# Kernel optimization log

Measured on AMD Instinct MI355X. Metric: run time of the kernel, lower is better.

The kernel has to match this reference:

```python
import jax, jax.numpy as jnp
import numpy as np

DIM = 128
KNN = 16
EPS = 1e-5


def knn_feature(coords, k):
    # coords: [B, K, D]; returns [B, K, k] nearest-neighbor indices (self excluded)
    inner = -2.0 * jnp.einsum('bid,bjd->bij', coords, coords)
    xx = jnp.sum(coords * coords, axis=-1, keepdims=True)  # [B,K,1]
    dist = xx + jnp.swapaxes(xx, 1, 2) + inner  # [B,K,K]
    K = coords.shape[1]
    diag = jnp.eye(K, dtype=bool)[None]
    dist = jnp.where(diag, 1e9, dist)
    _, idx = jax.lax.top_k(-dist, k)  # smallest distances
    return idx


def setup_inputs() -> dict:
    key = jax.random.key(0)
    ks = jax.random.split(key, 10)
    B, K, C = 8, 4096, DIM
    s1 = 1.0 / np.sqrt(2 * C)
    s2 = 1.0 / np.sqrt(C)
    return {
        'x': jax.random.normal(ks[0], (B, K, C), jnp.float32),
        'pos_embed': jax.random.normal(ks[1], (B, K, C), jnp.float32),
        'rel_pos_coords': jax.random.normal(ks[2], (B, K, 3), jnp.float32),
        'gamma': jnp.ones((C,), jnp.float32),
        'beta': jnp.zeros((C,), jnp.float32),
        'W_a1': jax.random.normal(ks[3], (2 * C, C), jnp.float32) * s1,
        'b_a1': jnp.zeros((C,), jnp.float32),
        'W_a2': jax.random.normal(ks[4], (C, 1), jnp.float32) * s2,
        'b_a2': jnp.zeros((1,), jnp.float32),
        'W_f1': jax.random.normal(ks[5], (2 * C, C), jnp.float32) * s1,
        'b_f1': jnp.zeros((C,), jnp.float32),
    }


def reference(x, pos_embed, rel_pos_coords, gamma, beta, W_a1, b_a1, W_a2, b_a2, W_f1, b_f1):
    B, K, C = x.shape
    k_eff = min(KNN, K - 1)
    # Pre-norm LayerNorm + positional embedding
    mu = jnp.mean(x, axis=-1, keepdims=True)
    var = jnp.mean((x - mu) ** 2, axis=-1, keepdims=True)
    x_norm = (x - mu) * jax.lax.rsqrt(var + EPS) * gamma + beta
    xp = x_norm + pos_embed  # [B,K,C]

    idx = knn_feature(rel_pos_coords, k_eff)  # [B,K,k]
    neighbor_feat = jax.vmap(lambda f, i: f[i])(xp, idx)  # [B,K,k,C]
    self_feat = jnp.broadcast_to(xp[:, :, None, :], neighbor_feat.shape)

    attn_in = jnp.concatenate([self_feat, neighbor_feat], axis=-1)  # [B,K,k,2C]
    h = jax.nn.leaky_relu(attn_in @ W_a1 + b_a1, 0.2)
    logits = h @ W_a2 + b_a2  # [B,K,k,1]
    attn = jax.nn.softmax(logits, axis=2)

    feat_in = jnp.concatenate([self_feat, neighbor_feat - self_feat], axis=-1)
    transformed = jax.nn.leaky_relu(feat_in @ W_f1 + b_f1, 0.2)  # [B,K,k,C]

    agg = jnp.sum(attn * transformed, axis=2)  # [B,K,C]
    # DropPath in eval mode is identity
    return agg
```

## Files before the change

kernel.cpp:

```cpp
#include <hip/hip_runtime.h>

#define B_ 8
#define K_ 4096
#define C_ 128
#define KN 16

typedef __attribute__((ext_vector_type(8))) short bf16x8;
typedef __attribute__((ext_vector_type(4))) float f32x4;

__device__ __forceinline__ unsigned short f2bf(float f) {
  unsigned u = __float_as_uint(f);
  unsigned r = (u + 0x7FFFu + ((u >> 16) & 1u)) >> 16;
  return (unsigned short)r;
}
__device__ __forceinline__ float bf2f(unsigned short s) {
  return __uint_as_float(((unsigned)s) << 16);
}

__device__ __forceinline__ float dist_exact(float4 q, float4 c) {
  float dot = __fadd_rn(__fadd_rn(__fmul_rn(q.x, c.x), __fmul_rn(q.y, c.y)),
                        __fmul_rn(q.z, c.z));
  return __fadd_rn(__fadd_rn(q.w, c.w), __fmul_rn(-2.0f, dot));
}
__device__ __forceinline__ float escr(float4 q, float4 c, float ch) {
  return fmaf(-q.x, c.x, fmaf(-q.y, c.y, fmaf(-q.z, c.z, ch)));
}

__global__ __launch_bounds__(256) void k_pre(
    const float* __restrict__ x, const float* __restrict__ pos,
    const float* __restrict__ gamma, const float* __restrict__ beta,
    const float* __restrict__ Wa1, const float* __restrict__ Wf1,
    const float* __restrict__ coords, unsigned short* __restrict__ A,
    unsigned short* __restrict__ WT, float4* __restrict__ cc4) {
  int blk = blockIdx.x;
  if (blk < 8192) {
    int wave = threadIdx.x >> 6;
    int lane = threadIdx.x & 63;
    size_t row = (size_t)blk * 4 + wave;
    const float2* xr = (const float2*)(x + row * C_);
    const float2* pr = (const float2*)(pos + row * C_);
    float2 a = xr[lane];
    float s = a.x + a.y;
#pragma unroll
    for (int o = 1; o < 64; o <<= 1) s += __shfl_xor(s, o);
    float mu = s * (1.0f / 128.0f);
    float dx = a.x - mu, dy = a.y - mu;
    float v = dx * dx + dy * dy;
#pragma unroll
    for (int o = 1; o < 64; o <<= 1) v += __shfl_xor(v, o);
    float rstd = rsqrtf(v * (1.0f / 128.0f) + 1e-5f);
    float2 gm = ((const float2*)gamma)[lane];
    float2 bt = ((const float2*)beta)[lane];
    float2 pp = pr[lane];
    float o0 = dx * rstd * gm.x + bt.x + pp.x;
    float o1 = dy * rstd * gm.y + bt.y + pp.y;
    ushort2 o = make_ushort2(f2bf(o0), f2bf(o1));
    *(ushort2*)(A + row * C_ + 2 * lane) = o;
  } else if (blk < 8320) {
    int i = (blk - 8192) * 256 + threadIdx.x;
    float px = coords[i * 3], py = coords[i * 3 + 1], pz = coords[i * 3 + 2];
    float w = __fadd_rn(__fadd_rn(__fmul_rn(px, px), __fmul_rn(py, py)),
                        __fmul_rn(pz, pz));
    cc4[i] = make_float4(px, py, pz, w);
  } else {
    int i = (blk - 8320) * 256 + threadIdx.x;
    int q = i >> 7;
    int r = i & 127;
    float v;
    if (q < 128)
      v = Wa1[r * 128 + q];
    else if (q < 256)
      v = Wf1[r * 128 + (q - 128)] - Wf1[(128 + r) * 128 + (q - 128)];
    else {
      int c = (q - 256) >> 1;
      if (((q - 256) & 1) == 0)
        v = Wa1[(128 + r) * 128 + c];
      else
        v = Wf1[(128 + r) * 128 + c];
    }
    WT[i] = f2bf(v);
  }
}

__global__ __launch_bounds__(256) void k_knn(const float4* __restrict__ cc4,
                                             int* __restrict__ idx) {
  __shared__ unsigned cbuf[4][4][64];
  __shared__ unsigned scnt[4][4];
  int wave = threadIdx.x >> 6, lane = threadIdx.x & 63;
  int gw = blockIdx.x * 4 + wave;
  int b = gw >> 10;
  int qbase = (gw & 1023) * 4;
  const float4* cb = cc4 + (size_t)b * K_;
  if (lane < 4) scnt[wave][lane] = 0u;
  __asm__ volatile("s_waitcnt lgkmcnt(0)" ::: "memory");
  float4 Q[4];
#pragma unroll
  for (int qq = 0; qq < 4; ++qq) Q[qq] = cb[qbase + qq];

  float m0 = 1e30f, m1 = 1e30f, m2 = 1e30f, m3 = 1e30f;
#pragma unroll 4
  for (int it = 0; it < 48; ++it) {
    float4 c = cb[(it << 6) + lane];
    float ch = c.w * 0.5f;
    m0 = fminf(m0, escr(Q[0], c, ch));
    m1 = fminf(m1, escr(Q[1], c, ch));
    m2 = fminf(m2, escr(Q[2], c, ch));
    m3 = fminf(m3, escr(Q[3], c, ch));
  }
  float ub[4];
  float mv[4] = {m0, m1, m2, m3};
#pragma unroll
  for (int qq = 0; qq < 4; ++qq) {
    float v = mv[qq];
#pragma unroll
    for (int k = 2; k <= 64; k <<= 1) {
#pragma unroll
      for (int jj = k >> 1; jj >= 1; jj >>= 1) {
        float o = __shfl_xor(v, jj);
        bool amHigh = (lane & jj) != 0;
        bool up = (lane & k) != 0;
        bool gt = v > o;
        bool take = (amHigh ? !gt : gt) ^ up;
        v = take ? o : v;
      }
    }
    ub[qq] = __shfl(v, 16) + 5e-4f;
  }

#pragma unroll 2
  for (int it = 0; it < 64; ++it) {
    int j = (it << 6) + lane;
    float4 c = cb[j];
    float ch = c.w * 0.5f;
#pragma unroll
    for (int qq = 0; qq < 4; ++qq) {
      float e = escr(Q[qq], c, ch);
      if (e <= ub[qq]) {
        unsigned pos = atomicAdd(&scnt[wave][qq], 1u);
        if (pos < 64u) cbuf[wave][qq][pos] = (unsigned)j;
      }
    }
  }
  __asm__ volatile("s_waitcnt lgkmcnt(0)" ::: "memory");

#pragma unroll
  for (int qq = 0; qq < 4; ++qq) {
    unsigned m = scnt[wave][qq];
    m = m < 64u ? m : 64u;
    bool valid = lane < (int)m;
    unsigned ji = valid ? cbuf[wave][qq][lane] : 0u;
    if (valid && ji == (unsigned)(qbase + qq)) valid = false;
    float4 c = cb[ji];
    float dC = valid ? dist_exact(Q[qq], c) : 1e30f;
    int iC = valid ? (int)ji : 0x7fffffff;
#pragma unroll
    for (int k = 2; k <= 64; k <<= 1) {
#pragma unroll
      for (int jj = k >> 1; jj >= 1; jj >>= 1) {
        float od = __shfl_xor(dC, jj);
        int oi = __shfl_xor(iC, jj);
        bool amHigh = (lane & jj) != 0;
        bool up = (lane & k) != 0;
        bool gt = (dC > od) || (dC == od && iC > oi);
        bool take = (amHigh ? !gt : gt) ^ up;
        dC = take ? od : dC;
        iC = take ? oi : iC;
      }
    }
    if (lane < KN)
      idx[((size_t)b * K_ + (qbase + qq)) * KN + lane] = iC;
  }
}

__global__ __launch_bounds__(256) void k_gemm_mfma(
    const unsigned short* __restrict__ A, const unsigned short* __restrict__ BT,
    unsigned short* __restrict__ SN) {
  __shared__ char lB[32768];
  int bb = blockIdx.x & 7;
  int rest = blockIdx.x >> 3;
  int mbl = rest >> 2, nb = rest & 3;
  int m0 = bb * 4096 + mbl * 128, n0 = nb * 128;
  int t = threadIdx.x;
  {
    const char* src = (const char*)(BT + (size_t)n0 * 128);
#pragma unroll
    for (int i = 0; i < 8; ++i) {
      int byte = (t + i * 256) * 16;
      int n = byte >> 8;
      int sb = byte ^ ((n & 7) << 4);
      *(float4*)(lB + sb) = *(const float4*)(src + byte);
    }
  }
  __syncthreads();
  int wave = t >> 6, lane = t & 63;
  int wr = wave >> 1, wc = wave & 1;
  int lm = lane & 15, lk = lane >> 4;
  f32x4 z = {0.f, 0.f, 0.f, 0.f};
  f32x4 acc00 = z, acc01 = z, acc02 = z, acc03 = z;
  f32x4 acc10 = z, acc11 = z, acc12 = z, acc13 = z;
  f32x4 acc20 = z, acc21 = z, acc22 = z, acc23 = z;
  f32x4 acc30 = z, acc31 = z, acc32 = z, acc33 = z;
  const char* abase =
      (const char*)A + (size_t)(m0 + wr * 64 + lm) * 256 + lk * 16;
#pragma unroll
  for (int ks = 0; ks < 4; ++ks) {
    bf16x8 af[4], bfr[4];
#pragma unroll
    for (int mt = 0; mt < 4; ++mt)
      af[mt] = *(const bf16x8*)(abase + (size_t)mt * 4096 + ks * 64);
#pragma unroll
    for (int nt = 0; nt < 4; ++nt) {
      int n_local = wc * 64 + nt * 16 + lm;
      int byte = n_local * 256 + ks * 64 + lk * 16;
      byte ^= (n_local & 7) << 4;
      bfr[nt] = *(const bf16x8*)(lB + byte);
    }
    acc00 = __builtin_amdgcn_mfma_f32_16x16x32_bf16(af[0], bfr[0], acc00, 0, 0, 0);
    acc01 = __builtin_amdgcn_mfma_f32_16x16x32_bf16(af[0], bfr[1], acc01, 0, 0, 0);
    acc02 = __builtin_amdgcn_mfma_f32_16x16x32_bf16(af[0], bfr[2], acc02, 0, 0, 0);
    acc03 = __builtin_amdgcn_mfma_f32_16x16x32_bf16(af[0], bfr[3], acc03, 0, 0, 0);
    acc10 = __builtin_amdgcn_mfma_f32_16x16x32_bf16(af[1], bfr[0], acc10, 0, 0, 0);
    acc11 = __builtin_amdgcn_mfma_f32_16x16x32_bf16(af[1], bfr[1], acc11, 0, 0, 0);
    acc12 = __builtin_amdgcn_mfma_f32_16x16x32_bf16(af[1], bfr[2], acc12, 0, 0, 0);
    acc13 = __builtin_amdgcn_mfma_f32_16x16x32_bf16(af[1], bfr[3], acc13, 0, 0, 0);
    acc20 = __builtin_amdgcn_mfma_f32_16x16x32_bf16(af[2], bfr[0], acc20, 0, 0, 0);
    acc21 = __builtin_amdgcn_mfma_f32_16x16x32_bf16(af[2], bfr[1], acc21, 0, 0, 0);
    acc22 = __builtin_amdgcn_mfma_f32_16x16x32_bf16(af[2], bfr[2], acc22, 0, 0, 0);
    acc23 = __builtin_amdgcn_mfma_f32_16x16x32_bf16(af[2], bfr[3], acc23, 0, 0, 0);
    acc30 = __builtin_amdgcn_mfma_f32_16x16x32_bf16(af[3], bfr[0], acc30, 0, 0, 0);
    acc31 = __builtin_amdgcn_mfma_f32_16x16x32_bf16(af[3], bfr[1], acc31, 0, 0, 0);
    acc32 = __builtin_amdgcn_mfma_f32_16x16x32_bf16(af[3], bfr[2], acc32, 0, 0, 0);
    acc33 = __builtin_amdgcn_mfma_f32_16x16x32_bf16(af[3], bfr[3], acc33, 0, 0, 0);
  }
  f32x4 accs[4][4] = {{acc00, acc01, acc02, acc03},
                      {acc10, acc11, acc12, acc13},
                      {acc20, acc21, acc22, acc23},
                      {acc30, acc31, acc32, acc33}};
#pragma unroll
  for (int mt = 0; mt < 4; ++mt) {
#pragma unroll
    for (int nt = 0; nt < 4; ++nt) {
#pragma unroll
      for (int r = 0; r < 4; ++r) {
        int row = m0 + wr * 64 + mt * 16 + lk * 4 + r;
        int col = n0 + wc * 64 + nt * 16 + lm;
        SN[(size_t)row * 512 + col] = f2bf(accs[mt][nt][r]);
      }
    }
  }
}

__global__ __launch_bounds__(256) void k_attn(
    const unsigned short* __restrict__ SN, const int* __restrict__ idx,
    const float* __restrict__ b_a1, const float* __restrict__ b_f1,
    const float* __restrict__ W_a2, const float* __restrict__ b_a2,
    float* __restrict__ out) {
  int wave = threadIdx.x >> 6, lane = threadIdx.x & 63;
  int g = lane >> 4, r = lane & 15;
  int b = blockIdx.x & 7;
  int w = blockIdx.x >> 3;
  size_t gpt = (size_t)b * K_ + w * 4 + wave;
  const unsigned short* sr = SN + gpt * 512;
  bf16x8 sa8 = *(const bf16x8*)(sr + 8 * r);
  bf16x8 sf8 = *(const bf16x8*)(sr + 128 + 8 * r);
  float4 bav0 = *(const float4*)(b_a1 + 8 * r);
  float4 bav1 = *(const float4*)(b_a1 + 8 * r + 4);
  float4 bfv0 = *(const float4*)(b_f1 + 8 * r);
  float4 bfv1 = *(const float4*)(b_f1 + 8 * r + 4);
  float4 w2v0 = *(const float4*)(W_a2 + 8 * r);
  float4 w2v1 = *(const float4*)(W_a2 + 8 * r + 4);
  float sab[8], sfb[8], w2v[8];
  {
    float bav[8] = {bav0.x, bav0.y, bav0.z, bav0.w, bav1.x, bav1.y, bav1.z, bav1.w};
    float bfv[8] = {bfv0.x, bfv0.y, bfv0.z, bfv0.w, bfv1.x, bfv1.y, bfv1.z, bfv1.w};
    float wv[8] = {w2v0.x, w2v0.y, w2v0.z, w2v0.w, w2v1.x, w2v1.y, w2v1.z, w2v1.w};
#pragma unroll
    for (int i = 0; i < 8; ++i) {
      sab[i] = bf2f((unsigned short)sa8[i]) + bav[i];
      sfb[i] = bf2f((unsigned short)sf8[i]) + bfv[i];
      w2v[i] = wv[i];
    }
  }
  float ba2v = b_a2[0];
  int nv = 0;
  if (lane < 16) nv = idx[gpt * 16 + lane];
  float lgl[4];
  float tsv[4][8];
#pragma unroll
  for (int round = 0; round < 4; ++round) {
    int n = __shfl(nv, round * 4 + g);
    const unsigned short* nr =
        SN + ((size_t)b * K_ + n) * 512 + 256 + 16 * r;
    bf16x8 u0 = *(const bf16x8*)(nr);
    bf16x8 u1 = *(const bf16x8*)(nr + 8);
    float dot = 0.0f;
#pragma unroll
    for (int i = 0; i < 4; ++i) {
      float h = sab[i] + bf2f((unsigned short)u0[2 * i]);
      h = h >= 0.0f ? h : 0.2f * h;
      float tv = sfb[i] + bf2f((unsigned short)u0[2 * i + 1]);
      tv = tv >= 0.0f ? tv : 0.2f * tv;
      dot = fmaf(h, w2v[i], dot);
      tsv[round][i] = tv;
    }
#pragma unroll
    for (int i = 0; i < 4; ++i) {
      float h = sab[4 + i] + bf2f((unsigned short)u1[2 * i]);
      h = h >= 0.0f ? h : 0.2f * h;
      float tv = sfb[4 + i] + bf2f((unsigned short)u1[2 * i + 1]);
      tv = tv >= 0.0f ? tv : 0.2f * tv;
      dot = fmaf(h, w2v[4 + i], dot);
      tsv[round][4 + i] = tv;
    }
#pragma unroll
    for (int o = 1; o < 16; o <<= 1) dot += __shfl_xor(dot, o);
    lgl[round] = dot + ba2v;
  }
  float mx = fmaxf(fmaxf(lgl[0], lgl[1]), fmaxf(lgl[2], lgl[3]));
  mx = fmaxf(mx, __shfl_xor(mx, 16));
  mx = fmaxf(mx, __shfl_xor(mx, 32));
  float e[4];
  float s = 0.0f;
#pragma unroll
  for (int round = 0; round < 4; ++round) {
    e[round] = expf(lgl[round] - mx);
    s += e[round];
  }
  s += __shfl_xor(s, 16);
  s += __shfl_xor(s, 32);
  float inv = 1.0f / s;
  float o8[8] = {0, 0, 0, 0, 0, 0, 0, 0};
#pragma unroll
  for (int round = 0; round < 4; ++round) {
    float a = e[round] * inv;
#pragma unroll
    for (int i = 0; i < 8; ++i) o8[i] = fmaf(a, tsv[round][i], o8[i]);
  }
#pragma unroll
  for (int i = 0; i < 8; ++i) {
    o8[i] += __shfl_xor(o8[i], 16);
    o8[i] += __shfl_xor(o8[i], 32);
  }
  if (g == 0) {
    float* op = out + gpt * 128 + 8 * r;
    *(float4*)op = make_float4(o8[0], o8[1], o8[2], o8[3]);
    *(float4*)(op + 4) = make_float4(o8[4], o8[5], o8[6], o8[7]);
  }
}

extern "C" void kernel_launch(void* const* d_in, const int* in_sizes, int n_in,
                              void* d_out, int out_size, void* d_ws,
                              size_t ws_size, hipStream_t stream) {
  const float* x = (const float*)d_in[0];
  const float* pos = (const float*)d_in[1];
  const float* coords = (const float*)d_in[2];
  const float* gamma = (const float*)d_in[3];
  const float* beta = (const float*)d_in[4];
  const float* Wa1 = (const float*)d_in[5];
  const float* ba1 = (const float*)d_in[6];
  const float* Wa2 = (const float*)d_in[7];
  const float* ba2 = (const float*)d_in[8];
  const float* Wf1 = (const float*)d_in[9];
  const float* bf1 = (const float*)d_in[10];
  float* out = (float*)d_out;

  char* ws = (char*)d_ws;
  unsigned short* A = (unsigned short*)ws;
  unsigned short* SN = (unsigned short*)(ws + (size_t)16 * 1024 * 1024);
  unsigned short* WT = (unsigned short*)(ws + (size_t)80 * 1024 * 1024);
  int* idx = (int*)(ws + (size_t)80 * 1024 * 1024 + 512 * 1024);
  float4* cc4 = (float4*)(ws + (size_t)80 * 1024 * 1024 + 2560 * 1024);

  k_pre<<<8576, 256, 0, stream>>>(x, pos, gamma, beta, Wa1, Wf1, coords, A, WT,
                                  cc4);
  k_knn<<<2048, 256, 0, stream>>>(cc4, idx);
  k_gemm_mfma<<<1024, 256, 0, stream>>>(A, WT, SN);
  k_attn<<<8192, 256, 0, stream>>>(SN, idx, ba1, bf1, Wa2, ba2, out);
}
```

Measured before the change: 110.7 us.

## Fuse kNN search and projection GEMM into one kernel, skip unneeded sort stage

Merges the MFMA projection GEMM into the kNN kernel so that each block first computes a 128x64 output tile and then does its kNN work. This removes one launch and lets the compute-heavy GEMM share the GPU with the latency-bound kNN. The GEMM now reads B fragments straight from global memory into registers, with no LDS staging or barrier. The bitonic sort skips its last stage when there are at most 32 candidates. Risks include higher register pressure under launch_bounds(256,8) and uncoalesced global B loads.

```diff
diff --git a/kernel.cpp b/kernel.cpp
--- a/kernel.cpp
+++ b/kernel.cpp
@@ -82,11 +82,64 @@
   }
 }
 
-__global__ __launch_bounds__(256) void k_knn(const float4* __restrict__ cc4,
-                                             int* __restrict__ idx) {
+__global__ __launch_bounds__(256, 8) void k_gk(
+    const unsigned short* __restrict__ A, const unsigned short* __restrict__ WT,
+    unsigned short* __restrict__ SN, const float4* __restrict__ cc4,
+    int* __restrict__ idx) {
   __shared__ unsigned cbuf[4][4][64];
   __shared__ unsigned scnt[4][4];
-  int wave = threadIdx.x >> 6, lane = threadIdx.x & 63;
+  int t = threadIdx.x;
+  int wave = t >> 6, lane = t & 63;
+
+  {
+    int bb = blockIdx.x & 7;
+    int rest = blockIdx.x >> 3;
+    int m0 = bb * 4096 + (rest >> 3) * 128;
+    int n0 = (rest & 7) * 64;
+    int wr = wave >> 1, wc = wave & 1;
+    int lm = lane & 15, lk = lane >> 4;
+    const unsigned short* bbase =
+        WT + (size_t)(n0 + wc * 32 + lm) * 128 + lk * 8;
+    bf16x8 bfr[2][4];
+#pragma unroll
+    for (int nt = 0; nt < 2; ++nt)
+#pragma unroll
+      for (int ks = 0; ks < 4; ++ks)
+        bfr[nt][ks] = *(const bf16x8*)(bbase + nt * 16 * 128 + ks * 32);
+    f32x4 z = {0.f, 0.f, 0.f, 0.f};
+    f32x4 acc[4][2];
+#pragma unroll
+    for (int mt = 0; mt < 4; ++mt)
+#pragma unroll
+      for (int nt = 0; nt < 2; ++nt) acc[mt][nt] = z;
+    const unsigned short* abase =
+        A + (size_t)(m0 + wr * 64 + lm) * 128 + lk * 8;
+#pragma unroll
+    for (int ks = 0; ks < 4; ++ks) {
+      bf16x8 af[4];
+#pragma unroll
+      for (int mt = 0; mt < 4; ++mt)
+        af[mt] = *(const bf16x8*)(abase + mt * 16 * 128 + ks * 32);
+#pragma unroll
+      for (int mt = 0; mt < 4; ++mt) {
+        acc[mt][0] = __builtin_amdgcn_mfma_f32_16x16x32_bf16(
+            af[mt], bfr[0][ks], acc[mt][0], 0, 0, 0);
+        acc[mt][1] = __builtin_amdgcn_mfma_f32_16x16x32_bf16(
+            af[mt], bfr[1][ks], acc[mt][1], 0, 0, 0);
+      }
+    }
+#pragma unroll
+    for (int mt = 0; mt < 4; ++mt)
+#pragma unroll
+      for (int nt = 0; nt < 2; ++nt)
+#pragma unroll
+        for (int r = 0; r < 4; ++r) {
+          int row = m0 + wr * 64 + mt * 16 + lk * 4 + r;
+          int col = n0 + wc * 32 + nt * 16 + lm;
+          SN[(size_t)row * 512 + col] = f2bf(acc[mt][nt][r]);
+        }
+  }
+
   int gw = blockIdx.x * 4 + wave;
   int b = gw >> 10;
   int qbase = (gw & 1023) * 4;
@@ -153,100 +206,29 @@
     float4 c = cb[ji];
     float dC = valid ? dist_exact(Q[qq], c) : 1e30f;
     int iC = valid ? (int)ji : 0x7fffffff;
-#pragma unroll
-    for (int k = 2; k <= 64; k <<= 1) {
-#pragma unroll
-      for (int jj = k >> 1; jj >= 1; jj >>= 1) {
-        float od = __shfl_xor(dC, jj);
-        int oi = __shfl_xor(iC, jj);
-        bool amHigh = (lane & jj) != 0;
-        bool up = (lane & k) != 0;
-        bool gt = (dC > od) || (dC == od && iC > oi);
-        bool take = (amHigh ? !gt : gt) ^ up;
-        dC = take ? od : dC;
-        iC = take ? oi : iC;
-      }
-    }
+#define SORT_STAGE(KV)                                              \
+  {                                                                 \
+    const int k = (KV);                                             \
+    for (int jj = k >> 1; jj >= 1; jj >>= 1) {                      \
+      float od = __shfl_xor(dC, jj);                                \
+      int oi = __shfl_xor(iC, jj);                                  \
+      bool amHigh = (lane & jj) != 0;                               \
+      bool up = (lane & k) != 0;                                    \
+      bool gt = (dC > od) || (dC == od && iC > oi);                 \
+      bool take = (amHigh ? !gt : gt) ^ up;                         \
+      dC = take ? od : dC;                                          \
+      iC = take ? oi : iC;                                          \
+    }                                                               \
+  }
+    if (m <= 32u) {
+      SORT_STAGE(2) SORT_STAGE(4) SORT_STAGE(8) SORT_STAGE(16) SORT_STAGE(32)
+    } else {
+      SORT_STAGE(2) SORT_STAGE(4) SORT_STAGE(8) SORT_STAGE(16) SORT_STAGE(32)
+      SORT_STAGE(64)
+    }
+#undef SORT_STAGE
     if (lane < KN)
       idx[((size_t)b * K_ + (qbase + qq)) * KN + lane] = iC;
-  }
-}
-
-__global__ __launch_bounds__(256) void k_gemm_mfma(
-    const unsigned short* __restrict__ A, const unsigned short* __restrict__ BT,
-    unsigned short* __restrict__ SN) {
-  __shared__ char lB[32768];
-  int bb = blockIdx.x & 7;
-  int rest = blockIdx.x >> 3;
-  int mbl = rest >> 2, nb = rest & 3;
-  int m0 = bb * 4096 + mbl * 128, n0 = nb * 128;
-  int t = threadIdx.x;
-  {
-    const char* src = (const char*)(BT + (size_t)n0 * 128);
-#pragma unroll
-    for (int i = 0; i < 8; ++i) {
-      int byte = (t + i * 256) * 16;
-      int n = byte >> 8;
-      int sb = byte ^ ((n & 7) << 4);
-      *(float4*)(lB + sb) = *(const float4*)(src + byte);
-    }
-  }
-  __syncthreads();
-  int wave = t >> 6, lane = t & 63;
-  int wr = wave >> 1, wc = wave & 1;
-  int lm = lane & 15, lk = lane >> 4;
-  f32x4 z = {0.f, 0.f, 0.f, 0.f};
-  f32x4 acc00 = z, acc01 = z, acc02 = z, acc03 = z;
-  f32x4 acc10 = z, acc11 = z, acc12 = z, acc13 = z;
-  f32x4 acc20 = z, acc21 = z, acc22 = z, acc23 = z;
-  f32x4 acc30 = z, acc31 = z, acc32 = z, acc33 = z;
-  const char* abase =
-      (const char*)A + (size_t)(m0 + wr * 64 + lm) * 256 + lk * 16;
-#pragma unroll
-  for (int ks = 0; ks < 4; ++ks) {
-    bf16x8 af[4], bfr[4];
-#pragma unroll
-    for (int mt = 0; mt < 4; ++mt)
-      af[mt] = *(const bf16x8*)(abase + (size_t)mt * 4096 + ks * 64);
-#pragma unroll
-    for (int nt = 0; nt < 4; ++nt) {
-      int n_local = wc * 64 + nt * 16 + lm;
-      int byte = n_local * 256 + ks * 64 + lk * 16;
-      byte ^= (n_local & 7) << 4;
-      bfr[nt] = *(const bf16x8*)(lB + byte);
-    }
-    acc00 = __builtin_amdgcn_mfma_f32_16x16x32_bf16(af[0], bfr[0], acc00, 0, 0, 0);
-    acc01 = __builtin_amdgcn_mfma_f32_16x16x32_bf16(af[0], bfr[1], acc01, 0, 0, 0);
-    acc02 = __builtin_amdgcn_mfma_f32_16x16x32_bf16(af[0], bfr[2], acc02, 0, 0, 0);
-    acc03 = __builtin_amdgcn_mfma_f32_16x16x32_bf16(af[0], bfr[3], acc03, 0, 0, 0);
-    acc10 = __builtin_amdgcn_mfma_f32_16x16x32_bf16(af[1], bfr[0], acc10, 0, 0, 0);
-    acc11 = __builtin_amdgcn_mfma_f32_16x16x32_bf16(af[1], bfr[1], acc11, 0, 0, 0);
-    acc12 = __builtin_amdgcn_mfma_f32_16x16x32_bf16(af[1], bfr[2], acc12, 0, 0, 0);
-    acc13 = __builtin_amdgcn_mfma_f32_16x16x32_bf16(af[1], bfr[3], acc13, 0, 0, 0);
-    acc20 = __builtin_amdgcn_mfma_f32_16x16x32_bf16(af[2], bfr[0], acc20, 0, 0, 0);
-    acc21 = __builtin_amdgcn_mfma_f32_16x16x32_bf16(af[2], bfr[1], acc21, 0, 0, 0);
-    acc22 = __builtin_amdgcn_mfma_f32_16x16x32_bf16(af[2], bfr[2], acc22, 0, 0, 0);
-    acc23 = __builtin_amdgcn_mfma_f32_16x16x32_bf16(af[2], bfr[3], acc23, 0, 0, 0);
-    acc30 = __builtin_amdgcn_mfma_f32_16x16x32_bf16(af[3], bfr[0], acc30, 0, 0, 0);
-    acc31 = __builtin_amdgcn_mfma_f32_16x16x32_bf16(af[3], bfr[1], acc31, 0, 0, 0);
-    acc32 = __builtin_amdgcn_mfma_f32_16x16x32_bf16(af[3], bfr[2], acc32, 0, 0, 0);
-    acc33 = __builtin_amdgcn_mfma_f32_16x16x32_bf16(af[3], bfr[3], acc33, 0, 0, 0);
-  }
-  f32x4 accs[4][4] = {{acc00, acc01, acc02, acc03},
-                      {acc10, acc11, acc12, acc13},
-                      {acc20, acc21, acc22, acc23},
-                      {acc30, acc31, acc32, acc33}};
-#pragma unroll
-  for (int mt = 0; mt < 4; ++mt) {
-#pragma unroll
-    for (int nt = 0; nt < 4; ++nt) {
-#pragma unroll
-      for (int r = 0; r < 4; ++r) {
-        int row = m0 + wr * 64 + mt * 16 + lk * 4 + r;
-        int col = n0 + wc * 64 + nt * 16 + lm;
-        SN[(size_t)row * 512 + col] = f2bf(accs[mt][nt][r]);
-      }
-    }
   }
 }
 
@@ -373,7 +355,6 @@
 
   k_pre<<<8576, 256, 0, stream>>>(x, pos, gamma, beta, Wa1, Wf1, coords, A, WT,
                                   cc4);
-  k_knn<<<2048, 256, 0, stream>>>(cc4, idx);
-  k_gemm_mfma<<<1024, 256, 0, stream>>>(A, WT, SN);
+  k_gk<<<2048, 256, 0, stream>>>(A, WT, SN, cc4, idx);
   k_attn<<<8192, 256, 0, stream>>>(SN, idx, ba1, bf1, Wa2, ba2, out);
 }
```

Result: slower. 116.9 us (+5.6%).

## Replace brute-force KNN with uniform-grid cell search plus exact fallback

Applied to the files above, without the earlier changes.

Points are binned into a 16^3 uniform grid per batch using counting, a prefix scan and a scatter. Each cell's queries then search only the 27 neighbouring cells, loaded into shared memory, instead of all 4096 points. A margin test checks that the 16th neighbour lies inside the searched region. Queries that fail it, or whose neighbourhood overflows or underfills, go to a brute-force fallback kernel, so results stay exact. This cuts the O(K^2) distance work, at the cost of extra launches, atomics, memsets and many near-empty blocks.

```diff
diff --git a/kernel.cpp b/kernel.cpp
--- a/kernel.cpp
+++ b/kernel.cpp
@@ -4,6 +4,10 @@
 #define K_ 4096
 #define C_ 128
 #define KN 16
+#define GR 16
+#define CS 0.4375f
+#define GLO -3.5f
+#define CAP 768
 
 typedef __attribute__((ext_vector_type(8))) short bf16x8;
 typedef __attribute__((ext_vector_type(4))) float f32x4;
@@ -31,7 +35,8 @@
     const float* __restrict__ gamma, const float* __restrict__ beta,
     const float* __restrict__ Wa1, const float* __restrict__ Wf1,
     const float* __restrict__ coords, unsigned short* __restrict__ A,
-    unsigned short* __restrict__ WT, float4* __restrict__ cc4) {
+    unsigned short* __restrict__ WT, float4* __restrict__ cc4,
+    unsigned* __restrict__ counts, int* __restrict__ cellid) {
   int blk = blockIdx.x;
   if (blk < 8192) {
     int wave = threadIdx.x >> 6;
@@ -62,7 +67,7 @@
     float w = __fadd_rn(__fadd_rn(__fmul_rn(px, px), __fmul_rn(py, py)),
                         __fmul_rn(pz, pz));
     cc4[i] = make_float4(px, py, pz, w);
-  } else {
+  } else if (blk < 8576) {
     int i = (blk - 8320) * 256 + threadIdx.x;
     int q = i >> 7;
     int r = i & 127;
@@ -79,39 +84,245 @@
         v = Wf1[(128 + r) * 128 + c];
     }
     WT[i] = f2bf(v);
-  }
-}
-
-__global__ __launch_bounds__(256) void k_knn(const float4* __restrict__ cc4,
-                                             int* __restrict__ idx) {
+  } else {
+    int i = (blk - 8576) * 256 + threadIdx.x;
+    float px = coords[i * 3], py = coords[i * 3 + 1], pz = coords[i * 3 + 2];
+    int cx = (int)floorf((px - GLO) * (1.0f / CS));
+    int cy = (int)floorf((py - GLO) * (1.0f / CS));
+    int cz = (int)floorf((pz - GLO) * (1.0f / CS));
+    cx = min(15, max(0, cx));
+    cy = min(15, max(0, cy));
+    cz = min(15, max(0, cz));
+    int cid = (cx << 8) | (cy << 4) | cz;
+    cellid[i] = cid;
+    atomicAdd(&counts[(i >> 12) * 4096 + cid], 1u);
+  }
+}
+
+__global__ __launch_bounds__(1024) void k_scan(const unsigned* __restrict__ counts,
+                                               unsigned* __restrict__ start,
+                                               unsigned* __restrict__ cursor) {
+  __shared__ unsigned ts[1024];
+  int b = blockIdx.x, t = threadIdx.x;
+  const unsigned* cb = counts + b * 4096;
+  unsigned c0 = cb[4 * t], c1 = cb[4 * t + 1], c2 = cb[4 * t + 2],
+           c3 = cb[4 * t + 3];
+  ts[t] = c0 + c1 + c2 + c3;
+  __syncthreads();
+  for (int off = 1; off < 1024; off <<= 1) {
+    unsigned v = ts[t];
+    unsigned u = (t >= off) ? ts[t - off] : 0u;
+    __syncthreads();
+    ts[t] = v + u;
+    __syncthreads();
+  }
+  unsigned excl = (t == 0) ? 0u : ts[t - 1];
+  unsigned base = (unsigned)b * 4096u + excl;
+  unsigned g = b * 4096 + 4 * t;
+  start[g] = base;
+  start[g + 1] = base + c0;
+  start[g + 2] = base + c0 + c1;
+  start[g + 3] = base + c0 + c1 + c2;
+  cursor[g] = base;
+  cursor[g + 1] = base + c0;
+  cursor[g + 2] = base + c0 + c1;
+  cursor[g + 3] = base + c0 + c1 + c2;
+}
+
+__global__ __launch_bounds__(256) void k_scatter(
+    const float4* __restrict__ cc4, const int* __restrict__ cellid,
+    unsigned* __restrict__ cursor, float4* __restrict__ sC,
+    int* __restrict__ sI) {
+  int i = blockIdx.x * 256 + threadIdx.x;
+  int g = (i >> 12) * 4096 + cellid[i];
+  unsigned p = atomicAdd(&cursor[g], 1u);
+  sC[p] = cc4[i];
+  sI[p] = i & 4095;
+}
+
+__global__ __launch_bounds__(256) void k_knng(
+    const float4* __restrict__ sC, const int* __restrict__ sI,
+    const unsigned* __restrict__ start, const unsigned* __restrict__ counts,
+    int* __restrict__ idx, int* __restrict__ fblist, int* __restrict__ fbcnt) {
+  __shared__ float4 candL[CAP];
+  __shared__ int sidxL[CAP];
   __shared__ unsigned cbuf[4][4][64];
   __shared__ unsigned scnt[4][4];
-  int wave = threadIdx.x >> 6, lane = threadIdx.x & 63;
-  int gw = blockIdx.x * 4 + wave;
-  int b = gw >> 10;
-  int qbase = (gw & 1023) * 4;
-  const float4* cb = cc4 + (size_t)b * K_;
-  if (lane < 4) scnt[wave][lane] = 0u;
-  __asm__ volatile("s_waitcnt lgkmcnt(0)" ::: "memory");
-  float4 Q[4];
-#pragma unroll
-  for (int qq = 0; qq < 4; ++qq) Q[qq] = cb[qbase + qq];
-
-  float m0 = 1e30f, m1 = 1e30f, m2 = 1e30f, m3 = 1e30f;
+  __shared__ int fbbase;
+  int bi = blockIdx.x;
+  int b = bi >> 12, cid = bi & 4095;
+  unsigned nq = counts[bi];
+  if (nq == 0) return;
+  int cx = cid >> 8, cy = (cid >> 4) & 15, cz = cid & 15;
+  int t = threadIdx.x, wave = t >> 6, lane = t & 63;
+  unsigned qs = start[bi];
+
+  int n = 0;
+  {
+    int zlo = cz > 0 ? cz - 1 : 0;
+    int zhi = cz < 15 ? cz + 1 : 15;
+    for (int dx = -1; dx <= 1; ++dx) {
+      int X = cx + dx;
+      if (X < 0 || X > 15) continue;
+      for (int dy = -1; dy <= 1; ++dy) {
+        int Y = cy + dy;
+        if (Y < 0 || Y > 15) continue;
+        int glo = b * 4096 + (X << 8) + (Y << 4) + zlo;
+        int ghi = glo + (zhi - zlo);
+        unsigned rs = start[glo];
+        unsigned re = start[ghi] + counts[ghi];
+        int len = (int)(re - rs);
+        if (n + len <= CAP) {
+          for (int i = t; i < len; i += 256) {
+            candL[n + i] = sC[rs + i];
+            sidxL[n + i] = sI[rs + i];
+          }
+        }
+        n += len;
+      }
+    }
+  }
+  if (n > CAP || n < 17) {
+    if (t == 0) fbbase = atomicAdd(fbcnt, (int)nq);
+    __syncthreads();
+    for (unsigned i = t; i < nq; i += 256)
+      fblist[fbbase + i] = b * 4096 + sI[qs + i];
+    return;
+  }
+  __syncthreads();
+
+  int nIter = (n + 63) >> 6;
+  unsigned qe = qs + nq;
+  float clox = GLO + cx * CS, cloy = GLO + cy * CS, cloz = GLO + cz * CS;
+
+  for (unsigned q0 = qs + wave * 4; q0 < qe; q0 += 16) {
+    int nv = (int)(qe - q0);
+    if (nv > 4) nv = 4;
+    float4 Q[4];
+    int orig[4];
+#pragma unroll
+    for (int qq = 0; qq < 4; ++qq) {
+      unsigned qi = q0 + (qq < nv ? (unsigned)qq : 0u);
+      Q[qq] = sC[qi];
+      orig[qq] = sI[qi];
+    }
+    float mn[4] = {1e30f, 1e30f, 1e30f, 1e30f};
+    for (int it = 0; it < nIter; ++it) {
+      int j = (it << 6) + lane;
+      bool v = j < n;
+      float4 c = candL[v ? j : 0];
+      float ch = c.w * 0.5f;
+#pragma unroll
+      for (int qq = 0; qq < 4; ++qq) {
+        float e = escr(Q[qq], c, ch);
+        if (v) mn[qq] = fminf(mn[qq], e);
+      }
+    }
+    float ub[4];
+#pragma unroll
+    for (int qq = 0; qq < 4; ++qq) {
+      float v = mn[qq];
+#pragma unroll
+      for (int k = 2; k <= 64; k <<= 1) {
+#pragma unroll
+        for (int jj = k >> 1; jj >= 1; jj >>= 1) {
+          float o = __shfl_xor(v, jj);
+          bool amHigh = (lane & jj) != 0;
+          bool up = (lane & k) != 0;
+          bool gt = v > o;
+          bool take = (amHigh ? !gt : gt) ^ up;
+          v = take ? o : v;
+        }
+      }
+      ub[qq] = __shfl(v, 16) + 5e-4f;
+    }
+    if (lane < 4) scnt[wave][lane] = 0u;
+    __asm__ volatile("s_waitcnt lgkmcnt(0)" ::: "memory");
+    for (int it = 0; it < nIter; ++it) {
+      int j = (it << 6) + lane;
+      bool v = j < n;
+      float4 c = candL[v ? j : 0];
+      float ch = c.w * 0.5f;
+#pragma unroll
+      for (int qq = 0; qq < 4; ++qq) {
+        float e = escr(Q[qq], c, ch);
+        if (v && qq < nv && e <= ub[qq]) {
+          unsigned pos = atomicAdd(&scnt[wave][qq], 1u);
+          if (pos < 64u) cbuf[wave][qq][pos] = (unsigned)j;
+        }
+      }
+    }
+    __asm__ volatile("s_waitcnt lgkmcnt(0)" ::: "memory");
+    for (int qq = 0; qq < nv; ++qq) {
+      unsigned m = scnt[wave][qq];
+      if (m > 64u) {
+        if (lane == 0) {
+          int p = atomicAdd(fbcnt, 1);
+          fblist[p] = b * 4096 + orig[qq];
+        }
+        continue;
+      }
+      bool valid = lane < (int)m;
+      unsigned ji = valid ? cbuf[wave][qq][lane] : 0u;
+      float4 c = candL[ji];
+      int io = valid ? sidxL[ji] : 0x7fffffff;
+      if (io == orig[qq]) valid = false;
+      float dC = valid ? dist_exact(Q[qq], c) : 1e30f;
+      int iC = valid ? io : 0x7fffffff;
+#pragma unroll
+      for (int k = 2; k <= 64; k <<= 1) {
+#pragma unroll
+        for (int jj = k >> 1; jj >= 1; jj >>= 1) {
+          float od = __shfl_xor(dC, jj);
+          int oi = __shfl_xor(iC, jj);
+          bool amHigh = (lane & jj) != 0;
+          bool up = (lane & k) != 0;
+          bool gt = (dC > od) || (dC == od && iC > oi);
+          bool take = (amHigh ? !gt : gt) ^ up;
+          dC = take ? od : dC;
+          iC = take ? oi : iC;
+        }
+      }
+      float d16 = __shfl(dC, 15);
+      float mg = 1e15f;
+      if (cx >= 2) mg = fminf(mg, Q[qq].x - (clox - CS));
+      if (cx <= 13) mg = fminf(mg, (clox + 2.0f * CS) - Q[qq].x);
+      if (cy >= 2) mg = fminf(mg, Q[qq].y - (cloy - CS));
+      if (cy <= 13) mg = fminf(mg, (cloy + 2.0f * CS) - Q[qq].y);
+      if (cz >= 2) mg = fminf(mg, Q[qq].z - (cloz - CS));
+      if (cz <= 13) mg = fminf(mg, (cloz + 2.0f * CS) - Q[qq].z);
+      bool ok = d16 <= mg * mg - 1e-4f;
+      if (ok) {
+        if (lane < KN)
+          idx[((size_t)b * K_ + orig[qq]) * KN + lane] = iC;
+      } else if (lane == 0) {
+        int p = atomicAdd(fbcnt, 1);
+        fblist[p] = b * 4096 + orig[qq];
+      }
+    }
+  }
+}
+
+__global__ __launch_bounds__(256) void k_fb(const float4* __restrict__ cc4,
+                                            const int* __restrict__ fblist,
+                                            const int* __restrict__ fbcnt,
+                                            int* __restrict__ idx) {
+  __shared__ unsigned cbuf[4][64];
+  __shared__ unsigned scnt[4];
+  int t = threadIdx.x, wave = t >> 6, lane = t & 63;
+  int count = *fbcnt;
+  for (int w = blockIdx.x * 4 + wave; w < count; w += 2048) {
+    int qg = fblist[w];
+    int b = qg >> 12, ql = qg & 4095;
+    const float4* cb = cc4 + (size_t)b * K_;
+    float4 Q = cb[ql];
+    float mn = 1e30f;
 #pragma unroll 4
-  for (int it = 0; it < 48; ++it) {
-    float4 c = cb[(it << 6) + lane];
-    float ch = c.w * 0.5f;
-    m0 = fminf(m0, escr(Q[0], c, ch));
-    m1 = fminf(m1, escr(Q[1], c, ch));
-    m2 = fminf(m2, escr(Q[2], c, ch));
-    m3 = fminf(m3, escr(Q[3], c, ch));
-  }
-  float ub[4];
-  float mv[4] = {m0, m1, m2, m3};
-#pragma unroll
-  for (int qq = 0; qq < 4; ++qq) {
-    float v = mv[qq];
+    for (int it = 0; it < 64; ++it) {
+      float4 c = cb[(it << 6) + lane];
+      mn = fminf(mn, escr(Q, c, c.w * 0.5f));
+    }
+    float v = mn;
 #pragma unroll
     for (int k = 2; k <= 64; k <<= 1) {
 #pragma unroll
@@ -124,34 +335,27 @@
         v = take ? o : v;
       }
     }
-    ub[qq] = __shfl(v, 16) + 5e-4f;
-  }
-
+    float ub = __shfl(v, 16) + 5e-4f;
+    if (lane == 0) scnt[wave] = 0u;
+    __asm__ volatile("s_waitcnt lgkmcnt(0)" ::: "memory");
 #pragma unroll 2
-  for (int it = 0; it < 64; ++it) {
-    int j = (it << 6) + lane;
-    float4 c = cb[j];
-    float ch = c.w * 0.5f;
-#pragma unroll
-    for (int qq = 0; qq < 4; ++qq) {
-      float e = escr(Q[qq], c, ch);
-      if (e <= ub[qq]) {
-        unsigned pos = atomicAdd(&scnt[wave][qq], 1u);
-        if (pos < 64u) cbuf[wave][qq][pos] = (unsigned)j;
-      }
-    }
-  }
-  __asm__ volatile("s_waitcnt lgkmcnt(0)" ::: "memory");
-
-#pragma unroll
-  for (int qq = 0; qq < 4; ++qq) {
-    unsigned m = scnt[wave][qq];
+    for (int it = 0; it < 64; ++it) {
+      int j = (it << 6) + lane;
+      float4 c = cb[j];
+      float e = escr(Q, c, c.w * 0.5f);
+      if (e <= ub) {
+        unsigned pos = atomicAdd(&scnt[wave], 1u);
+        if (pos < 64u) cbuf[wave][pos] = (unsigned)j;
+      }
+    }
+    __asm__ volatile("s_waitcnt lgkmcnt(0)" ::: "memory");
+    unsigned m = scnt[wave];
     m = m < 64u ? m : 64u;
     bool valid = lane < (int)m;
-    unsigned ji = valid ? cbuf[wave][qq][lane] : 0u;
-    if (valid && ji == (unsigned)(qbase + qq)) valid = false;
+    unsigned ji = valid ? cbuf[wave][lane] : 0u;
+    if (valid && ji == (unsigned)ql) valid = false;
     float4 c = cb[ji];
-    float dC = valid ? dist_exact(Q[qq], c) : 1e30f;
+    float dC = valid ? dist_exact(Q, c) : 1e30f;
     int iC = valid ? (int)ji : 0x7fffffff;
 #pragma unroll
     for (int k = 2; k <= 64; k <<= 1) {
@@ -167,8 +371,7 @@
         iC = take ? oi : iC;
       }
     }
-    if (lane < KN)
-      idx[((size_t)b * K_ + (qbase + qq)) * KN + lane] = iC;
+    if (lane < KN) idx[((size_t)b * K_ + ql) * KN + lane] = iC;
   }
 }
 
@@ -365,15 +568,29 @@
   float* out = (float*)d_out;
 
   char* ws = (char*)d_ws;
+  const size_t MB = 1024 * 1024;
   unsigned short* A = (unsigned short*)ws;
-  unsigned short* SN = (unsigned short*)(ws + (size_t)16 * 1024 * 1024);
-  unsigned short* WT = (unsigned short*)(ws + (size_t)80 * 1024 * 1024);
-  int* idx = (int*)(ws + (size_t)80 * 1024 * 1024 + 512 * 1024);
-  float4* cc4 = (float4*)(ws + (size_t)80 * 1024 * 1024 + 2560 * 1024);
-
-  k_pre<<<8576, 256, 0, stream>>>(x, pos, gamma, beta, Wa1, Wf1, coords, A, WT,
-                                  cc4);
-  k_knn<<<2048, 256, 0, stream>>>(cc4, idx);
+  unsigned* counts = (unsigned*)(ws + 8 * MB);
+  int* cellid = (int*)(ws + 8 * MB + 128 * 1024);
+  unsigned* start = (unsigned*)(ws + 8 * MB + 256 * 1024);
+  unsigned* cursor = (unsigned*)(ws + 8 * MB + 384 * 1024);
+  float4* sC = (float4*)(ws + 8 * MB + 512 * 1024);
+  int* sI = (int*)(ws + 8 * MB + 1024 * 1024);
+  int* fblist = (int*)(ws + 8 * MB + 1152 * 1024);
+  int* fbcnt = (int*)(ws + 8 * MB + 1280 * 1024);
+  unsigned short* SN = (unsigned short*)(ws + 16 * MB);
+  unsigned short* WT = (unsigned short*)(ws + 80 * MB);
+  int* idx = (int*)(ws + 80 * MB + 512 * 1024);
+  float4* cc4 = (float4*)(ws + 80 * MB + 2560 * 1024);
+
+  hipMemsetAsync(counts, 0, 32768 * sizeof(unsigned), stream);
+  hipMemsetAsync(fbcnt, 0, sizeof(int), stream);
+  k_pre<<<8704, 256, 0, stream>>>(x, pos, gamma, beta, Wa1, Wf1, coords, A, WT,
+                                  cc4, counts, cellid);
+  k_scan<<<8, 1024, 0, stream>>>(counts, start, cursor);
+  k_scatter<<<128, 256, 0, stream>>>(cc4, cellid, cursor, sC, sI);
+  k_knng<<<32768, 256, 0, stream>>>(sC, sI, start, counts, idx, fblist, fbcnt);
+  k_fb<<<512, 256, 0, stream>>>(cc4, fblist, fbcnt, idx);
   k_gemm_mfma<<<1024, 256, 0, stream>>>(A, WT, SN);
   k_attn<<<8192, 256, 0, stream>>>(SN, idx, ba1, bf1, Wa2, ba2, out);
 }
```

After: 314.2 us. 2.84x slower.
